# Performance work log

Hardware: AMD Instinct MI355X
Metric: run time of the kernel (lower is better)

## Reference

```python
import jax, jax.numpy as jnp
import numpy as np
from jax import lax

B, N, T, D = 16, 307, 48, 128
H, DK = 8, 16          # nb_head, d_k = d_model // nb_head
K = 3                  # kernel_size
PAD = K - 1
SEGS = (12, 12, 24)    # w_length, d_length, h_length
SCALE = 1.0 / float(np.sqrt(DK))


def _causal_conv_proj(x, w, b):
    """x: (B, N, Ts, D) -> (B, N, H, Ts, DK) via causal Conv2d((1,K)) along time."""
    xc = x.transpose(0, 3, 1, 2)  # (B, D, N, Ts)
    y = lax.conv_general_dilated(
        xc, w, window_strides=(1, 1), padding=[(0, 0), (PAD, PAD)],
        dimension_numbers=("NCHW", "OIHW", "NCHW"))
    y = y[..., :-PAD] + b[None, :, None, None]          # trim right pad -> causal
    b_, _, n_, t_ = y.shape
    # view(B, H, DK, N, Ts).permute(0, 3, 1, 4, 2)
    return y.reshape(b_, H, DK, n_, t_).transpose(0, 3, 1, 4, 2)


def setup_inputs() -> dict:
    rng = jax.random.key(0)
    ks = jax.random.split(rng, 11)
    s = 0.05
    mask = jnp.broadcast_to(jnp.tril(jnp.ones((T, T), jnp.int32)), (B, T, T))
    return {
        "query": jax.random.normal(ks[0], (B, N, T, D), jnp.float32),
        "key": jax.random.normal(ks[1], (B, N, T, D), jnp.float32),
        "value": jax.random.normal(ks[2], (B, N, T, D), jnp.float32),
        "mask": mask,
        "conv_q_w": jax.random.normal(ks[3], (D, D, 1, K), jnp.float32) * s,
        "conv_q_b": jax.random.normal(ks[4], (D,), jnp.float32) * s,
        "conv_k_w": jax.random.normal(ks[5], (D, D, 1, K), jnp.float32) * s,
        "conv_k_b": jax.random.normal(ks[6], (D,), jnp.float32) * s,
        "lin_v_w": jax.random.normal(ks[7], (D, D), jnp.float32) * s,
        "lin_v_b": jax.random.normal(ks[8], (D,), jnp.float32) * s,
        "lin_o_w": jax.random.normal(ks[9], (D, D), jnp.float32) * s,
        "lin_o_b": jax.random.normal(ks[10], (D,), jnp.float32) * s,
    }


def reference(query, key, value, mask,
              conv_q_w, conv_q_b, conv_k_w, conv_k_b,
              lin_v_w, lin_v_b, lin_o_w, lin_o_b):
    # query_multi_segment = key_multi_segment = True: causal conv per time segment
    offs = np.concatenate([[0], np.cumsum(SEGS)])
    q = jnp.concatenate(
        [_causal_conv_proj(query[:, :, offs[i]:offs[i + 1], :], conv_q_w, conv_q_b)
         for i in range(len(SEGS))], axis=3)                    # (B, N, H, T, DK)
    k = jnp.concatenate(
        [_causal_conv_proj(key[:, :, offs[i]:offs[i + 1], :], conv_k_w, conv_k_b)
         for i in range(len(SEGS))], axis=3)                    # (B, N, H, T, DK)
    # value projection: Linear then (B, N, T, H, DK) -> (B, N, H, T, DK)
    v = (jnp.einsum('bntd,ed->bnte', value, lin_v_w) + lin_v_b)
    v = v.reshape(B, N, T, H, DK).transpose(0, 1, 3, 2, 4)
    # masked scaled-dot-product attention
    scores = jnp.einsum('bnhtd,bnhsd->bnhts', q, k) * SCALE     # (B, N, H, T, T)
    scores = jnp.where(mask[:, None, None] == 0, -1e9, scores)
    p = jax.nn.softmax(scores, axis=-1)
    x = jnp.einsum('bnhts,bnhsd->bnhtd', p, v)
    x = x.transpose(0, 1, 3, 2, 4).reshape(B, N, T, H * DK)     # (B, N, T, D)
    return jnp.einsum('bntd,ed->bnte', x, lin_o_w) + lin_o_b
```

## Files before the change

kernel.cpp:

```cpp
#include <hip/hip_runtime.h>
#include <hip/hip_bf16.h>


typedef __attribute__((ext_vector_type(8))) short short8;
typedef __attribute__((ext_vector_type(4))) float floatx4;
typedef __attribute__((ext_vector_type(4))) unsigned short ushortx4;

#define MFMA16(a, b, c) __builtin_amdgcn_mfma_f32_16x16x32_bf16((a), (b), (c), 0, 0, 0)

__device__ __forceinline__ unsigned short f2bf(float x) {
  __hip_bfloat16 h = __float2bfloat16(x);
  return __builtin_bit_cast(unsigned short, h);
}

__device__ __forceinline__ int prow(int t) {
  return t + 2 + (t >= 12 ? 2 : 0) + (t >= 24 ? 2 : 0);
}

__device__ __forceinline__ short8 lds8(const __hip_bfloat16* p) {
  return *(const short8*)p;
}

__global__ void prep_weights(const float* __restrict__ wq,
                             const float* __restrict__ wk,
                             const float* __restrict__ vw,
                             const float* __restrict__ ow,
                             __hip_bfloat16* __restrict__ dst) {
  int i = blockIdx.x * 256 + threadIdx.x;
  float v;
  if (i < 98304) {
    int which = i / 49152;
    int r = i % 49152;
    int tap = r / 16384;
    int rr = r & 16383;
    int e = rr >> 7, d = rr & 127;
    const float* src = which ? wk : wq;
    v = src[e * 384 + d * 3 + tap];
  } else {
    int r = i - 98304;
    int j = r & 16383;
    v = (r >> 14) ? ow[j] : vw[j];
  }
  dst[i] = __float2bfloat16(v);
}

constexpr int XS = 136;
constexpr int VS = 56;
constexpr int WQ_OFF = 0;
constexpr int WK_OFF = 49152;
constexpr int VW_OFF = 98304;
constexpr int OW_OFF = 114688;

__device__ __forceinline__ void stage_load(const float* __restrict__ src,
                                           float4* r, int tid) {
  const float4* g = (const float4*)src;
  #pragma unroll
  for (int it = 0; it < 6; ++it) r[it] = g[tid + it * 256];
}

__device__ __forceinline__ void stage_write(const float4* r,
                                            __hip_bfloat16* sh, int tid) {
  #pragma unroll
  for (int it = 0; it < 6; ++it) {
    int c = tid + it * 256;
    int t = c >> 5;
    int col = (c & 31) * 4;
    float4 f = r[it];
    ushortx4 pk;
    pk[0] = f2bf(f.x); pk[1] = f2bf(f.y); pk[2] = f2bf(f.z); pk[3] = f2bf(f.w);
    *(ushortx4*)&sh[prow(t) * XS + col] = pk;
  }
}

__device__ __forceinline__ void conv_acc(const __hip_bfloat16* shx,
                                         const __hip_bfloat16* __restrict__ wt,
                                         floatx4 acc[3][2],
                                         int wv, int quad, int l16) {
  const int e0 = (wv * 2) * 16 + l16;
  const int e1 = (wv * 2 + 1) * 16 + l16;
  #pragma unroll
  for (int tap = 0; tap < 3; ++tap) {
    const __hip_bfloat16* W = wt + tap * 16384;
    const int sh = 2 - tap;
    #pragma unroll
    for (int ks = 0; ks < 4; ++ks) {
      int k0 = ks * 32 + quad * 8;
      short8 b0 = lds8(W + e0 * 128 + k0);
      short8 b1 = lds8(W + e1 * 128 + k0);
      #pragma unroll
      for (int mi = 0; mi < 3; ++mi) {
        int t = mi * 16 + l16;
        short8 a = lds8(&shx[(prow(t) - sh) * XS + k0]);
        acc[mi][0] = MFMA16(a, b0, acc[mi][0]);
        acc[mi][1] = MFMA16(a, b1, acc[mi][1]);
      }
    }
  }
}

__device__ __forceinline__ void conv_write(floatx4 acc[3][2],
                                           const float* __restrict__ bias,
                                           __hip_bfloat16* dst,
                                           int wv, int quad, int l16) {
  #pragma unroll
  for (int nti = 0; nti < 2; ++nti) {
    int e = (wv * 2 + nti) * 16 + l16;
    float bb = bias[e];
    #pragma unroll
    for (int mi = 0; mi < 3; ++mi) {
      int t0 = mi * 16 + quad * 4;
      #pragma unroll
      for (int r = 0; r < 4; ++r)
        dst[(t0 + r) * XS + e] = __float2bfloat16(acc[mi][nti][r] + bb);
    }
  }
}

__global__ __launch_bounds__(256, 3) void fused_attn(
    const float* __restrict__ gq, const float* __restrict__ gk,
    const float* __restrict__ gv,
    const __hip_bfloat16* __restrict__ wts,
    const float* __restrict__ cqb, const float* __restrict__ ckb,
    const float* __restrict__ vb, const float* __restrict__ ob,
    float* __restrict__ out) {
  __shared__ __align__(16) __hip_bfloat16 shA[54 * XS];
  __shared__ __align__(16) __hip_bfloat16 shB[54 * XS];
  __shared__ __align__(16) __hip_bfloat16 sh_vt[128 * VS];
  __shared__ __align__(16) __hip_bfloat16 sh_p[4 * 16 * 64];

  const int tid  = threadIdx.x;
  const int wv   = tid >> 6;
  const int lane = tid & 63;
  const int quad = lane >> 4;
  const int l16  = lane & 15;
  const long base = (long)blockIdx.x * (48 * 128);

  const __hip_bfloat16* wq_t = wts + WQ_OFF;
  const __hip_bfloat16* wk_t = wts + WK_OFF;
  const __hip_bfloat16* vw   = wts + VW_OFF;
  const __hip_bfloat16* ow   = wts + OW_OFF;

  if (tid < 204) {
    int b = tid >= 102;
    int i = b ? tid - 102 : tid;
    int pr = i / 17, pc = i % 17;
    int row = (pr >> 1) * 14 + (pr & 1);
    uint4 z = {0, 0, 0, 0};
    __hip_bfloat16* s = b ? shB : shA;
    *(uint4*)&s[row * XS + pc * 8] = z;
  }

  const int e0 = (wv * 2) * 16 + l16;
  const int e1 = (wv * 2 + 1) * 16 + l16;

  float4 rv[6];
  stage_load(gv + base, rv, tid);
  stage_write(rv, shA, tid);
  float4 rq[6];
  stage_load(gq + base, rq, tid);
  __syncthreads();

  floatx4 vacc[3][2] = {};
  #pragma unroll
  for (int ks = 0; ks < 4; ++ks) {
    int k0 = ks * 32 + quad * 8;
    short8 b0 = lds8(vw + e0 * 128 + k0);
    short8 b1 = lds8(vw + e1 * 128 + k0);
    #pragma unroll
    for (int mi = 0; mi < 3; ++mi) {
      int t = mi * 16 + l16;
      short8 a = lds8(&shA[prow(t) * XS + k0]);
      vacc[mi][0] = MFMA16(a, b0, vacc[mi][0]);
      vacc[mi][1] = MFMA16(a, b1, vacc[mi][1]);
    }
  }
  stage_write(rq, shB, tid);
  float4 rk[6];
  stage_load(gk + base, rk, tid);
  __syncthreads();

  #pragma unroll
  for (int nti = 0; nti < 2; ++nti) {
    int e = (wv * 2 + nti) * 16 + l16;
    float bv = vb[e];
    #pragma unroll
    for (int mi = 0; mi < 3; ++mi) {
      int t0 = mi * 16 + quad * 4;
      ushortx4 pk;
      #pragma unroll
      for (int r = 0; r < 4; ++r) pk[r] = f2bf(vacc[mi][nti][r] + bv);
      *(ushortx4*)&sh_vt[e * VS + t0] = pk;
    }
  }

  floatx4 qacc[3][2] = {};
  conv_acc(shB, wq_t, qacc, wv, quad, l16);
  stage_write(rk, shA, tid);
  __syncthreads();

  conv_write(qacc, cqb, shB, wv, quad, l16);

  floatx4 kacc[3][2] = {};
  conv_acc(shA, wk_t, kacc, wv, quad, l16);
  __syncthreads();

  conv_write(kacc, ckb, shA, wv, quad, l16);
  __syncthreads();

  {
    __hip_bfloat16* shp = sh_p + wv * (16 * 64);
    if (lane < 32) {
      int lt = lane >> 1;
      int cp = (6 + (lane & 1)) ^ (lt & 7);
      uint4 z = {0, 0, 0, 0};
      *(uint4*)&shp[lt * 64 + cp * 8] = z;
    }
    short8 zf = {0, 0, 0, 0, 0, 0, 0, 0};
    #pragma unroll
    for (int hi = 0; hi < 2; ++hi) {
      const int hq = (wv * 2 + hi) * 16;
      #pragma unroll
      for (int mi = 0; mi < 3; ++mi) {
        floatx4 s0 = {}, s1 = {}, s2 = {};
        short8 aq  = (quad < 2) ? lds8(&shB[(mi * 16 + l16) * XS + hq + quad * 8]) : zf;
        short8 bk0 = (quad < 2) ? lds8(&shA[(l16) * XS + hq + quad * 8]) : zf;
        short8 bk1 = (quad < 2) ? lds8(&shA[(16 + l16) * XS + hq + quad * 8]) : zf;
        short8 bk2 = (quad < 2) ? lds8(&shA[(32 + l16) * XS + hq + quad * 8]) : zf;
        s0 = MFMA16(aq, bk0, s0);
        s1 = MFMA16(aq, bk1, s1);
        s2 = MFMA16(aq, bk2, s2);
        const int tb = mi * 16 + quad * 4;
        #pragma unroll
        for (int r = 0; r < 4; ++r) {
          int t = tb + r;
          float v0 = (l16 <= t)      ? s0[r] * 0.25f : -1e30f;
          float v1 = (16 + l16 <= t) ? s1[r] * 0.25f : -1e30f;
          float v2 = (32 + l16 <= t) ? s2[r] * 0.25f : -1e30f;
          float mx = fmaxf(v0, fmaxf(v1, v2));
          #pragma unroll
          for (int d = 1; d < 16; d <<= 1) mx = fmaxf(mx, __shfl_xor(mx, d, 64));
          float p0 = __expf(v0 - mx), p1 = __expf(v1 - mx), p2 = __expf(v2 - mx);
          float sm = p0 + p1 + p2;
          #pragma unroll
          for (int d = 1; d < 16; d <<= 1) sm += __shfl_xor(sm, d, 64);
          float inv = __builtin_amdgcn_rcpf(sm);
          int lt = quad * 4 + r;
          int xr = lt & 7, lo = l16 & 7, hi8 = l16 >> 3, rowb = lt * 64;
          shp[rowb + (((0 + hi8) ^ xr) << 3) + lo] = __float2bfloat16(p0 * inv);
          shp[rowb + (((2 + hi8) ^ xr) << 3) + lo] = __float2bfloat16(p1 * inv);
          shp[rowb + (((4 + hi8) ^ xr) << 3) + lo] = __float2bfloat16(p2 * inv);
        }
        floatx4 x = {};
        #pragma unroll
        for (int ks = 0; ks < 2; ++ks) {
          int c = (ks * 4 + quad) ^ (l16 & 7);
          short8 ap = lds8(&shp[l16 * 64 + c * 8]);
          int sb = ks * 32 + quad * 8;
          short8 bvv = (sb < 48) ? lds8(&sh_vt[(hq + l16) * VS + sb]) : zf;
          x = MFMA16(ap, bvv, x);
        }
        #pragma unroll
        for (int r = 0; r < 4; ++r)
          shB[(tb + r) * XS + hq + l16] = __float2bfloat16(x[r]);
      }
    }
  }
  __syncthreads();

  {
    floatx4 acc[3][2] = {};
    #pragma unroll
    for (int ks = 0; ks < 4; ++ks) {
      int k0 = ks * 32 + quad * 8;
      short8 b0 = lds8(ow + e0 * 128 + k0);
      short8 b1 = lds8(ow + e1 * 128 + k0);
      #pragma unroll
      for (int mi = 0; mi < 3; ++mi) {
        short8 a = lds8(&shB[(mi * 16 + l16) * XS + k0]);
        acc[mi][0] = MFMA16(a, b0, acc[mi][0]);
        acc[mi][1] = MFMA16(a, b1, acc[mi][1]);
      }
    }
    float* op = out + base;
    #pragma unroll
    for (int nti = 0; nti < 2; ++nti) {
      int e = (wv * 2 + nti) * 16 + l16;
      float bo = ob[e];
      #pragma unroll
      for (int mi = 0; mi < 3; ++mi) {
        int t0 = mi * 16 + quad * 4;
        #pragma unroll
        for (int r = 0; r < 4; ++r)
          op[(t0 + r) * 128 + e] = acc[mi][nti][r] + bo;
      }
    }
  }
}

extern "C" void kernel_launch(void* const* d_in, const int* in_sizes, int n_in,
                              void* d_out, int out_size, void* d_ws, size_t ws_size,
                              hipStream_t stream) {
  (void)in_sizes; (void)n_in; (void)out_size; (void)ws_size;
  const float* query = (const float*)d_in[0];
  const float* key   = (const float*)d_in[1];
  const float* value = (const float*)d_in[2];
  const float* cqw = (const float*)d_in[4];
  const float* cqb = (const float*)d_in[5];
  const float* ckw = (const float*)d_in[6];
  const float* ckb = (const float*)d_in[7];
  const float* vw  = (const float*)d_in[8];
  const float* vb  = (const float*)d_in[9];
  const float* ow  = (const float*)d_in[10];
  const float* ob  = (const float*)d_in[11];

  __hip_bfloat16* wts = (__hip_bfloat16*)d_ws;

  prep_weights<<<dim3(512), 256, 0, stream>>>(cqw, ckw, vw, ow, wts);
  fused_attn<<<dim3(16 * 307), 256, 0, stream>>>(
      query, key, value, wts, cqb, ckb, vb, ob, (float*)d_out);
}
```

Baseline: 484.3 us.

## Keep V projection fragments in registers via lane shuffles instead of LDS

The V-projection result is no longer written to a transposed shared-memory buffer. Each wave packs its accumulator values to bf16 and redistributes them across lanes with shuffles, so they arrive directly in the B-fragment layout used by the P·V MFMA. Dropping the sh_vt buffer reduces LDS use, and the launch bound is raised from 3 to 4 blocks per CU to exploit that. In exchange it adds shuffle instructions and register pressure, and the tighter launch bound may cause spills.

```diff
diff --git a/kernel.cpp b/kernel.cpp
--- a/kernel.cpp
+++ b/kernel.cpp
@@ -5,6 +5,7 @@
 typedef __attribute__((ext_vector_type(8))) short short8;
 typedef __attribute__((ext_vector_type(4))) float floatx4;
 typedef __attribute__((ext_vector_type(4))) unsigned short ushortx4;
+typedef __attribute__((ext_vector_type(4))) unsigned int uintx4;
 
 #define MFMA16(a, b, c) __builtin_amdgcn_mfma_f32_16x16x32_bf16((a), (b), (c), 0, 0, 0)
 
@@ -45,7 +46,6 @@
 }
 
 constexpr int XS = 136;
-constexpr int VS = 56;
 constexpr int WQ_OFF = 0;
 constexpr int WK_OFF = 49152;
 constexpr int VW_OFF = 98304;
@@ -116,7 +116,7 @@
   }
 }
 
-__global__ __launch_bounds__(256, 3) void fused_attn(
+__global__ __launch_bounds__(256, 4) void fused_attn(
     const float* __restrict__ gq, const float* __restrict__ gk,
     const float* __restrict__ gv,
     const __hip_bfloat16* __restrict__ wts,
@@ -125,7 +125,6 @@
     float* __restrict__ out) {
   __shared__ __align__(16) __hip_bfloat16 shA[54 * XS];
   __shared__ __align__(16) __hip_bfloat16 shB[54 * XS];
-  __shared__ __align__(16) __hip_bfloat16 sh_vt[128 * VS];
   __shared__ __align__(16) __hip_bfloat16 sh_p[4 * 16 * 64];
 
   const int tid  = threadIdx.x;
@@ -177,21 +176,46 @@
   stage_write(rq, shB, tid);
   float4 rk[6];
   stage_load(gk + base, rk, tid);
-  __syncthreads();
-
-  #pragma unroll
-  for (int nti = 0; nti < 2; ++nti) {
-    int e = (wv * 2 + nti) * 16 + l16;
-    float bv = vb[e];
-    #pragma unroll
-    for (int mi = 0; mi < 3; ++mi) {
-      int t0 = mi * 16 + quad * 4;
-      ushortx4 pk;
-      #pragma unroll
-      for (int r = 0; r < 4; ++r) pk[r] = f2bf(vacc[mi][nti][r] + bv);
-      *(ushortx4*)&sh_vt[e * VS + t0] = pk;
-    }
-  }
+
+  short8 vfrag[2][2];
+  {
+    unsigned vpk[3][2][2];
+    #pragma unroll
+    for (int nti = 0; nti < 2; ++nti) {
+      float bv = vb[(wv * 2 + nti) * 16 + l16];
+      #pragma unroll
+      for (int mi = 0; mi < 3; ++mi) {
+        #pragma unroll
+        for (int rp = 0; rp < 2; ++rp) {
+          unsigned lo = f2bf(vacc[mi][nti][2 * rp] + bv);
+          unsigned up = f2bf(vacc[mi][nti][2 * rp + 1] + bv);
+          vpk[mi][nti][rp] = lo | (up << 16);
+        }
+      }
+    }
+    const int srcA = ((quad & 1) * 2) * 16 + l16;
+    const int srcB = ((quad & 1) * 2 + 1) * 16 + l16;
+    const bool topq = (quad >> 1) != 0;
+    #pragma unroll
+    for (int hi = 0; hi < 2; ++hi) {
+      uintx4 u0, u1;
+      #pragma unroll
+      for (int jh = 0; jh < 2; ++jh) {
+        int src = jh ? srcB : srcA;
+        #pragma unroll
+        for (int rp = 0; rp < 2; ++rp) {
+          unsigned a0 = (unsigned)__shfl((int)vpk[0][hi][rp], src, 64);
+          unsigned a1 = (unsigned)__shfl((int)vpk[1][hi][rp], src, 64);
+          unsigned a2 = (unsigned)__shfl((int)vpk[2][hi][rp], src, 64);
+          u0[jh * 2 + rp] = topq ? a1 : a0;
+          u1[jh * 2 + rp] = topq ? 0u : a2;
+        }
+      }
+      vfrag[hi][0] = __builtin_bit_cast(short8, u0);
+      vfrag[hi][1] = __builtin_bit_cast(short8, u1);
+    }
+  }
+  __syncthreads();
 
   floatx4 qacc[3][2] = {};
   conv_acc(shB, wq_t, qacc, wv, quad, l16);
@@ -255,9 +279,7 @@
         for (int ks = 0; ks < 2; ++ks) {
           int c = (ks * 4 + quad) ^ (l16 & 7);
           short8 ap = lds8(&shp[l16 * 64 + c * 8]);
-          int sb = ks * 32 + quad * 8;
-          short8 bvv = (sb < 48) ? lds8(&sh_vt[(hq + l16) * VS + sb]) : zf;
-          x = MFMA16(ap, bvv, x);
+          x = MFMA16(ap, vfrag[hi][ks], x);
         }
         #pragma unroll
         for (int r = 0; r < 4; ++r)
```

Result: no change. 489.8 us (+1.1%).
